# Optimization experiments

Hardware: AMD Instinct MI355X
Metric: run time of the kernel (lower is better)

Reference implementation:

```python
import jax, jax.numpy as jnp
import numpy as np
from jax import lax

NUM_PATCHES = 64   # FPS sample count K
PATCH_SIZE = 32    # KNN neighbors per patch


def setup_inputs() -> dict:
    key = jax.random.key(0)
    points = jax.random.normal(key, (16, 65536, 3), dtype=jnp.float32)
    return {"points": points}


def _fps(xyz, K):
    """Iterative farthest point sampling. xyz: [B,N,3] -> idx [B,K].
    Deterministic start at index 0 (reference for random_start_point)."""
    B, N, _ = xyz.shape
    start = jnp.zeros((B,), dtype=jnp.int32)
    min_d0 = jnp.full((B, N), jnp.finfo(xyz.dtype).max, xyz.dtype)

    def step(carry, _):
        min_d, last = carry
        last_pt = jnp.take_along_axis(xyz, last[:, None, None], axis=1)  # [B,1,3]
        d = jnp.sum((xyz - last_pt) ** 2, axis=-1)                       # [B,N]
        min_d = jnp.minimum(min_d, d)
        nxt = jnp.argmax(min_d, axis=1).astype(jnp.int32)
        return (min_d, nxt), last

    (_, _), idxs = lax.scan(step, (min_d0, start), None, length=K)  # [K,B]
    return jnp.transpose(idxs)  # [B,K]


def _knn_idx(centers, pts, K):
    """K nearest neighbors (sorted ascending by distance). centers [B,P,3], pts [B,N,3]."""
    c2 = jnp.sum(centers * centers, -1)[:, :, None]                 # [B,P,1]
    p2 = jnp.sum(pts * pts, -1)[:, None, :]                         # [B,1,N]
    d2 = c2 + p2 - 2.0 * jnp.einsum('bpc,bnc->bpn', centers, pts)   # [B,P,N]
    _, idx = lax.top_k(-d2, K)                                      # sorted nearest-first
    return idx


def reference(points):
    xyz = points[..., :3]
    fps_idx = _fps(xyz, NUM_PATCHES)                                  # [B,P]
    centers = jnp.take_along_axis(xyz, fps_idx[..., None], axis=1)    # [B,P,3]
    idx = _knn_idx(centers, xyz, PATCH_SIZE)                          # [B,P,K]
    patches = jax.vmap(lambda p, i: p[i])(points, idx)                # [B,P,K,C]
    patches = patches.at[..., :3].add(-centers[:, :, None, :])        # center xyz part
    return patches, centers
```

## Files before the change

kernel.cpp:

```cpp
#include <hip/hip_runtime.h>
#include <float.h>

#define BATCH 16
#define NPTS  65536
#define NP    64
#define PS    32
#define SLICES 4
#define SLICE_PTS (NPTS / SLICES)
#define CAP   256


__device__ __forceinline__ unsigned long long enc64(double d) {
    unsigned long long u = (unsigned long long)__double_as_longlong(d);
    return u ^ ((u >> 63) ? 0xFFFFFFFFFFFFFFFFull : 0x8000000000000000ull);
}
__device__ __forceinline__ unsigned enc32(float f) {
    unsigned u = __float_as_uint(f);
    return u ^ ((u >> 31) ? 0xFFFFFFFFu : 0x80000000u);
}
__device__ __forceinline__ float dec32(unsigned e) {
    unsigned u = (e & 0x80000000u) ? (e ^ 0x80000000u) : ~e;
    return __uint_as_float(u);
}

#define SENT 0xFFFFFFFFFFFFFFFFull

__global__ __launch_bounds__(256, 2)
void fps_kernel(const float* __restrict__ pts,
                float* __restrict__ centers,
                unsigned long long* __restrict__ slots)
{
#pragma clang fp contract(off)
    const int b  = blockIdx.x & 15;
    const int wg = blockIdx.x >> 4;
    const int t  = threadIdx.x;
    const float* __restrict__ P = pts + (size_t)b * NPTS * 3;

    float x[16], y[16], z[16];
    double md[16];
    const int gi0 = wg * 4096 + t;
#pragma unroll
    for (int k = 0; k < 16; ++k) {
        int i = gi0 + (k << 8);
        x[k] = P[3*i+0]; y[k] = P[3*i+1]; z[k] = P[3*i+2];
        md[k] = DBL_MAX;
    }

    double cx = (double)P[0], cy = (double)P[1], cz = (double)P[2];
    if (wg == 0 && t == 0) {
        float* c0 = centers + b * (NP*3);
        c0[0] = P[0]; c0[1] = P[1]; c0[2] = P[2];
    }

    __shared__ unsigned long long wbest[4];
    __shared__ unsigned long long skey[16];

    unsigned long long* slot_it = slots + (size_t)b * 63 * 16;

    for (int it = 0; it < NP - 1; ++it) {
        double bd = -1.0; int bi = 0;
#pragma unroll
        for (int k = 0; k < 16; ++k) {
            double dx = (double)x[k] - cx;
            double dy = (double)y[k] - cy;
            double dz = (double)z[k] - cz;
            double d  = (dx*dx + dy*dy) + dz*dz;
            double m  = fmin(md[k], d);
            md[k] = m;
            if (m > bd) { bd = m; bi = gi0 + (k << 8); }
        }
        unsigned long long db  = (unsigned long long)__double_as_longlong(bd);
        unsigned long long key = 0x8000000000000000ull
                               | (db & 0xFFFFFFFFFFFF0000ull)
                               | (unsigned long long)((~bi) & 0xFFFF);
#pragma unroll
        for (int off = 32; off > 0; off >>= 1) {
            unsigned long long o = __shfl_xor(key, off, 64);
            if (o > key) key = o;
        }
        if ((t & 63) == 0) wbest[t >> 6] = key;
        __syncthreads();
        if (t == 0) {
            unsigned long long k0 = wbest[0];
            if (wbest[1] > k0) k0 = wbest[1];
            if (wbest[2] > k0) k0 = wbest[2];
            if (wbest[3] > k0) k0 = wbest[3];
            __hip_atomic_store(slot_it + wg, k0, __ATOMIC_RELAXED, __HIP_MEMORY_SCOPE_AGENT);
        }
        if (t < 16) {
            unsigned long long v;
            v = __hip_atomic_load(slot_it + t, __ATOMIC_RELAXED, __HIP_MEMORY_SCOPE_AGENT);
            while (v == 0) {
                __builtin_amdgcn_s_sleep(1);
                v = __hip_atomic_load(slot_it + t, __ATOMIC_RELAXED, __HIP_MEMORY_SCOPE_AGENT);
            }
            skey[t] = v;
        }
        __syncthreads();
        unsigned long long bk = skey[0];
#pragma unroll
        for (int j = 1; j < 16; ++j) if (skey[j] > bk) bk = skey[j];
        int sel = (int)((~bk) & 0xFFFFull);
        cx = (double)P[3*sel+0]; cy = (double)P[3*sel+1]; cz = (double)P[3*sel+2];
        if (wg == 0 && t == 0) {
            float* c = centers + b*(NP*3) + (it+1)*3;
            c[0] = P[3*sel+0]; c[1] = P[3*sel+1]; c[2] = P[3*sel+2];
        }
        slot_it += 16;
    }
}

__global__ __launch_bounds__(256, 4)
void knn_pass(const float* __restrict__ pts,
              const float* __restrict__ centers,
              unsigned long long* __restrict__ gkeys)
{
    const int t    = threadIdx.x;
    const int lane = t & 63;
    const int wid  = t >> 6;
    const int b    = blockIdx.x & 15;
    const int w    = (blockIdx.x >> 4) & 15;
    const int s    = blockIdx.x >> 8;
    const float* __restrict__ P = pts + (size_t)b * NPTS * 3;
    const int sbase = s * SLICE_PTS;
    const float4* __restrict__ P4 = (const float4*)(P + 3 * sbase);

    float m2x[4], m2y[4], m2z[4], c2f[4];
#pragma unroll
    for (int g = 0; g < 4; ++g) {
        int c = b * NP + w * 4 + g;
        float cx = centers[3*c+0], cy = centers[3*c+1], cz = centers[3*c+2];
        c2f[g] = cx*cx + cy*cy + cz*cz;
        m2x[g] = -2.0f*cx; m2y[g] = -2.0f*cy; m2z[g] = -2.0f*cz;
    }

    union PoolKeys {
        unsigned pool[4][512];
        unsigned long long keys[4][CAP];
    };
    __shared__ PoolKeys pk;
    __shared__ float    theta4[4];
    __shared__ int      cnt4[4];
    __shared__ unsigned idxbuf[4][CAP];

    float s0[4], s1[4];
#pragma unroll
    for (int g = 0; g < 4; ++g) { s0[g] = FLT_MAX; s1[g] = FLT_MAX; }
    {
        float4 A = P4[3*t], B = P4[3*t+1], C = P4[3*t+2];
        for (int k = 0; k < SLICE_PTS/1024; ++k) {
            int vb = ((k+1) & 15)*768 + 3*t;
            float4 An = P4[vb], Bn = P4[vb+1], Cn = P4[vb+2];
            float qx[4] = {A.x, A.w, B.z, C.y};
            float qy[4] = {A.y, B.x, B.w, C.z};
            float qz[4] = {A.z, B.y, C.x, C.w};
#pragma unroll
            for (int j = 0; j < 4; ++j) {
                float px = qx[j], py = qy[j], pz = qz[j];
                float p2 = px*px + py*py + pz*pz;
#pragma unroll
                for (int g = 0; g < 4; ++g) {
                    float d2 = fmaf(m2x[g], px, fmaf(m2y[g], py, fmaf(m2z[g], pz, c2f[g]))) + p2;
                    s1[g] = __builtin_amdgcn_fmed3f(s0[g], s1[g], d2);
                    s0[g] = fminf(s0[g], d2);
                }
            }
            A = An; B = Bn; C = Cn;
        }
    }
#pragma unroll
    for (int g = 0; g < 4; ++g) {
        pk.pool[g][t]       = enc32(s0[g]);
        pk.pool[g][256 + t] = enc32(s1[g]);
    }
    if (t < 4) cnt4[t] = 0;
    __syncthreads();

    {
        const int g = wid;
        unsigned e[8];
#pragma unroll
        for (int j = 0; j < 8; ++j) e[j] = pk.pool[g][j * 64 + lane];
        unsigned ans = 0;
        for (int bit = 31; bit >= 0; --bit) {
            unsigned test = ans | ((1u << bit) - 1u);
            int cnt = 0;
#pragma unroll
            for (int j = 0; j < 8; ++j)
                cnt += (int)__popcll(__ballot(e[j] <= test));
            if (cnt < 32) ans |= (1u << bit);
        }
        if (lane == 0) theta4[g] = dec32(ans) + 4.0e-3f;
    }
    __syncthreads();
    float th[4];
#pragma unroll
    for (int g = 0; g < 4; ++g) th[g] = theta4[g];

    {
        float4 A = P4[3*t], B = P4[3*t+1], C = P4[3*t+2];
        for (int k = 0; k < SLICE_PTS/1024; ++k) {
            int vb = ((k+1) & 15)*768 + 3*t;
            float4 An = P4[vb], Bn = P4[vb+1], Cn = P4[vb+2];
            float qx[4] = {A.x, A.w, B.z, C.y};
            float qy[4] = {A.y, B.x, B.w, C.z};
            float qz[4] = {A.z, B.y, C.x, C.w};
            int ib = sbase + (k << 10) + (t << 2);
#pragma unroll
            for (int j = 0; j < 4; ++j) {
                float px = qx[j], py = qy[j], pz = qz[j];
                float p2 = px*px + py*py + pz*pz;
#pragma unroll
                for (int g = 0; g < 4; ++g) {
                    float d2 = fmaf(m2x[g], px, fmaf(m2y[g], py, fmaf(m2z[g], pz, c2f[g]))) + p2;
                    if (d2 <= th[g]) {
                        int pos = atomicAdd(&cnt4[g], 1);
                        if (pos < CAP) idxbuf[g][pos] = (unsigned)(ib + j);
                    }
                }
            }
            A = An; B = Bn; C = Cn;
        }
    }
    __syncthreads();

    {
        const int g = wid;
        int n = cnt4[g]; if (n > CAP) n = CAP;
        double cxd, cyd, czd, c2d;
        {
#pragma clang fp contract(off)
            cxd = -0.5*(double)m2x[g]; cyd = -0.5*(double)m2y[g]; czd = -0.5*(double)m2z[g];
            c2d = (cxd*cxd + cyd*cyd) + czd*czd;
        }
        unsigned long long rg[4];
#pragma unroll
        for (int j = 0; j < 4; ++j) {
            int p_ = lane + 64*j;
            if (p_ < n) {
                unsigned i = idxbuf[g][p_];
                double d2x;
                {
#pragma clang fp contract(off)
                    double px_ = (double)P[3*i+0];
                    double py_ = (double)P[3*i+1];
                    double pz_ = (double)P[3*i+2];
                    double p2_ = (px_*px_ + py_*py_) + pz_*pz_;
                    double dt_ = (cxd*px_ + cyd*py_) + czd*pz_;
                    d2x = (c2d + p2_) - 2.0*dt_;
                }
                rg[j] = (enc64(d2x) & 0xFFFFFFFFFFFF0000ull)
                      | (unsigned long long)(i & 0xFFFF);
                pk.keys[g][p_] = rg[j];
            } else rg[j] = SENT;
        }
        const int c = b * NP + w * 4 + g;
        int rk[4] = {0, 0, 0, 0};
        for (int p = 0; p < n; ++p) {
            unsigned long long kj = pk.keys[g][p];
            rk[0] += (kj < rg[0]);
            rk[1] += (kj < rg[1]);
            rk[2] += (kj < rg[2]);
            rk[3] += (kj < rg[3]);
        }
        unsigned long long* gout = gkeys + ((size_t)c * SLICES + s) * PS;
#pragma unroll
        for (int j = 0; j < 4; ++j)
            if (lane + 64*j < n && rk[j] < PS) gout[rk[j]] = rg[j];
    }
}

__global__ __launch_bounds__(256, 4)
void knn_merge(const float* __restrict__ pts,
               const float* __restrict__ centers,
               const unsigned long long* __restrict__ gkeys,
               float* __restrict__ patches)
{
    const int lane = threadIdx.x & 63;
    const int wid  = threadIdx.x >> 6;
    const int b    = blockIdx.x & 15;
    const int grp  = blockIdx.x >> 4;
    const int c    = b * NP + grp * 4 + wid;
    const float* __restrict__ P = pts + (size_t)b * NPTS * 3;

    __shared__ unsigned long long mk[4][SLICES*PS];

    unsigned long long rg0 = gkeys[(size_t)c * (SLICES*PS) + lane];
    unsigned long long rg1 = gkeys[(size_t)c * (SLICES*PS) + 64 + lane];
    mk[wid][lane]      = rg0;
    mk[wid][64 + lane] = rg1;

    int r0 = 0, r1 = 0;
#pragma unroll 4
    for (int p = 0; p < SLICES*PS; ++p) {
        unsigned long long kj = mk[wid][p];
        r0 += (kj < rg0);
        r1 += (kj < rg1);
    }

    const float cx = centers[3*c+0], cy = centers[3*c+1], cz = centers[3*c+2];
    if (r0 < PS) {
        int i = (int)(rg0 & 0xFFFFull);
        float* o = patches + (((size_t)c * PS) + r0) * 3;
        o[0] = P[3*i+0] - cx;
        o[1] = P[3*i+1] - cy;
        o[2] = P[3*i+2] - cz;
    }
    if (r1 < PS) {
        int i = (int)(rg1 & 0xFFFFull);
        float* o = patches + (((size_t)c * PS) + r1) * 3;
        o[0] = P[3*i+0] - cx;
        o[1] = P[3*i+1] - cy;
        o[2] = P[3*i+2] - cz;
    }
}

extern "C" void kernel_launch(void* const* d_in, const int* in_sizes, int n_in,
                              void* d_out, int out_size, void* d_ws, size_t ws_size,
                              hipStream_t stream)
{
    const float* pts = (const float*)d_in[0];
    float* out      = (float*)d_out;
    float* patches  = out;
    float* centers  = out + (size_t)BATCH*NP*PS*3;

    unsigned long long* slots = (unsigned long long*)d_ws;
    unsigned long long* gkeys = (unsigned long long*)((char*)d_ws + 131072);

    (void)hipMemsetAsync(d_ws, 0, (size_t)BATCH * 63 * 16 * sizeof(unsigned long long), stream);
    fps_kernel<<<dim3(256), dim3(256), 0, stream>>>(pts, centers, slots);
    knn_pass<<<dim3(1024), dim3(256), 0, stream>>>(pts, centers, gkeys);
    knn_merge<<<dim3(256), dim3(256), 0, stream>>>(pts, centers, gkeys, patches);
}
```

Baseline: 212.1 us.

## Fuse KNN merge into pass kernel via last-arriving-block atomic counter

Removes the separate knn_merge launch. The last of the four slice blocks for each (batch, center-group), detected with an atomic fetch-add counter, now merges the per-slice candidate keys and writes the centered patches. This saves one kernel launch and its dependency gap. In exchange it adds an atomic, an extra block barrier and more shared memory in the pass kernel, and the merge now relies on the acq_rel atomic to make the other blocks' global writes visible.

New measurement: 223.4 us. 1.05x slower.

```diff
diff --git a/kernel.cpp b/kernel.cpp
--- a/kernel.cpp
+++ b/kernel.cpp
@@ -8,6 +8,8 @@
 #define SLICES 4
 #define SLICE_PTS (NPTS / SLICES)
 #define CAP   256
+#define AGENT __HIP_MEMORY_SCOPE_AGENT
+
 
 
 __device__ __forceinline__ unsigned long long enc64(double d) {
@@ -85,14 +87,14 @@
             if (wbest[1] > k0) k0 = wbest[1];
             if (wbest[2] > k0) k0 = wbest[2];
             if (wbest[3] > k0) k0 = wbest[3];
-            __hip_atomic_store(slot_it + wg, k0, __ATOMIC_RELAXED, __HIP_MEMORY_SCOPE_AGENT);
+            __hip_atomic_store(slot_it + wg, k0, __ATOMIC_RELAXED, AGENT);
         }
         if (t < 16) {
             unsigned long long v;
-            v = __hip_atomic_load(slot_it + t, __ATOMIC_RELAXED, __HIP_MEMORY_SCOPE_AGENT);
+            v = __hip_atomic_load(slot_it + t, __ATOMIC_RELAXED, AGENT);
             while (v == 0) {
                 __builtin_amdgcn_s_sleep(1);
-                v = __hip_atomic_load(slot_it + t, __ATOMIC_RELAXED, __HIP_MEMORY_SCOPE_AGENT);
+                v = __hip_atomic_load(slot_it + t, __ATOMIC_RELAXED, AGENT);
             }
             skey[t] = v;
         }
@@ -111,9 +113,11 @@
 }
 
 __global__ __launch_bounds__(256, 4)
-void knn_pass(const float* __restrict__ pts,
-              const float* __restrict__ centers,
-              unsigned long long* __restrict__ gkeys)
+void knn_fused(const float* __restrict__ pts,
+               const float* __restrict__ centers,
+               float* __restrict__ patches,
+               int* __restrict__ cntmw,
+               unsigned long long* __restrict__ gkeys)
 {
     const int t    = threadIdx.x;
     const int lane = t & 63;
@@ -142,6 +146,8 @@
     __shared__ float    theta4[4];
     __shared__ int      cnt4[4];
     __shared__ unsigned idxbuf[4][CAP];
+    __shared__ unsigned long long mk[4][SLICES*PS];
+    __shared__ int amMerger;
 
     float s0[4], s1[4];
 #pragma unroll
@@ -268,50 +274,44 @@
         for (int j = 0; j < 4; ++j)
             if (lane + 64*j < n && rk[j] < PS) gout[rk[j]] = rg[j];
     }
-}
-
-__global__ __launch_bounds__(256, 4)
-void knn_merge(const float* __restrict__ pts,
-               const float* __restrict__ centers,
-               const unsigned long long* __restrict__ gkeys,
-               float* __restrict__ patches)
-{
-    const int lane = threadIdx.x & 63;
-    const int wid  = threadIdx.x >> 6;
-    const int b    = blockIdx.x & 15;
-    const int grp  = blockIdx.x >> 4;
-    const int c    = b * NP + grp * 4 + wid;
-    const float* __restrict__ P = pts + (size_t)b * NPTS * 3;
-
-    __shared__ unsigned long long mk[4][SLICES*PS];
-
-    unsigned long long rg0 = gkeys[(size_t)c * (SLICES*PS) + lane];
-    unsigned long long rg1 = gkeys[(size_t)c * (SLICES*PS) + 64 + lane];
-    mk[wid][lane]      = rg0;
-    mk[wid][64 + lane] = rg1;
-
-    int r0 = 0, r1 = 0;
+    __syncthreads();
+
+    if (t == 0) {
+        int old = __hip_atomic_fetch_add(cntmw + b*16 + w, 1, __ATOMIC_ACQ_REL, AGENT);
+        amMerger = (old == SLICES - 1);
+    }
+    __syncthreads();
+    if (amMerger) {
+        const int c = b * NP + w * 4 + wid;
+        const unsigned long long* gk = gkeys + (size_t)c * (SLICES*PS);
+        unsigned long long rg0 = gk[lane];
+        unsigned long long rg1 = gk[64 + lane];
+        mk[wid][lane]      = rg0;
+        mk[wid][64 + lane] = rg1;
+        int r0 = 0, r1 = 0;
 #pragma unroll 4
-    for (int p = 0; p < SLICES*PS; ++p) {
-        unsigned long long kj = mk[wid][p];
-        r0 += (kj < rg0);
-        r1 += (kj < rg1);
-    }
-
-    const float cx = centers[3*c+0], cy = centers[3*c+1], cz = centers[3*c+2];
-    if (r0 < PS) {
-        int i = (int)(rg0 & 0xFFFFull);
-        float* o = patches + (((size_t)c * PS) + r0) * 3;
-        o[0] = P[3*i+0] - cx;
-        o[1] = P[3*i+1] - cy;
-        o[2] = P[3*i+2] - cz;
-    }
-    if (r1 < PS) {
-        int i = (int)(rg1 & 0xFFFFull);
-        float* o = patches + (((size_t)c * PS) + r1) * 3;
-        o[0] = P[3*i+0] - cx;
-        o[1] = P[3*i+1] - cy;
-        o[2] = P[3*i+2] - cz;
+        for (int p = 0; p < SLICES*PS; ++p) {
+            unsigned long long kj = mk[wid][p];
+            r0 += (kj < rg0);
+            r1 += (kj < rg1);
+        }
+        const float cx_ = -0.5f * m2x[wid];
+        const float cy_ = -0.5f * m2y[wid];
+        const float cz_ = -0.5f * m2z[wid];
+        if (r0 < PS) {
+            int i = (int)(rg0 & 0xFFFFull);
+            float* o = patches + (((size_t)c * PS) + r0) * 3;
+            o[0] = P[3*i+0] - cx_;
+            o[1] = P[3*i+1] - cy_;
+            o[2] = P[3*i+2] - cz_;
+        }
+        if (r1 < PS) {
+            int i = (int)(rg1 & 0xFFFFull);
+            float* o = patches + (((size_t)c * PS) + r1) * 3;
+            o[0] = P[3*i+0] - cx_;
+            o[1] = P[3*i+1] - cy_;
+            o[2] = P[3*i+2] - cz_;
+        }
     }
 }
 
@@ -325,10 +325,10 @@
     float* centers  = out + (size_t)BATCH*NP*PS*3;
 
     unsigned long long* slots = (unsigned long long*)d_ws;
+    int* cntmw = (int*)((char*)d_ws + 129024);
     unsigned long long* gkeys = (unsigned long long*)((char*)d_ws + 131072);
 
-    (void)hipMemsetAsync(d_ws, 0, (size_t)BATCH * 63 * 16 * sizeof(unsigned long long), stream);
+    (void)hipMemsetAsync(d_ws, 0, 130048, stream);
     fps_kernel<<<dim3(256), dim3(256), 0, stream>>>(pts, centers, slots);
-    knn_pass<<<dim3(1024), dim3(256), 0, stream>>>(pts, centers, gkeys);
-    knn_merge<<<dim3(256), dim3(256), 0, stream>>>(pts, centers, gkeys, patches);
-}
+    knn_fused<<<dim3(1024), dim3(256), 0, stream>>>(pts, centers, patches, cntmw, gkeys);
+}
```
